# Optimization experiments

Hardware: AMD Instinct MI355X
Metric: run time of the kernel (lower is better)

## Reference

```python
import jax, jax.numpy as jnp
import numpy as np

H = 8
HID = 512
DH = HID // H
EPS = 1e-5


def _ln(x, g, b):
    mu = jnp.mean(x, axis=-1, keepdims=True)
    var = jnp.mean(jnp.square(x - mu), axis=-1, keepdims=True)
    return (x - mu) * jax.lax.rsqrt(var + EPS) * g + b


def setup_inputs() -> dict:
    key = jax.random.key(0)
    ks = jax.random.split(key, 40)
    L, M, P, D = 4096, 1024, 4096, 512

    def xav(k, shp):
        lim = np.sqrt(6.0 / (shp[0] + shp[1]))
        return jax.random.uniform(k, shp, jnp.float32, -lim, lim)

    inp = {
        'lncRNA_embedding': jax.random.normal(ks[0], (L, D), jnp.float32),
        'miRNA_embedding': jax.random.normal(ks[1], (M, D), jnp.float32),
        'protein_embedding': jax.random.normal(ks[2], (P, D), jnp.float32),
        'lncRNA_miRNA_matrix': jax.random.randint(ks[3], (L, M), 0, 2, jnp.int32),
        'protein_miRNA_matrix': jax.random.randint(ks[4], (P, M), 0, 2, jnp.int32),
    }
    names = ['Wl', 'Wm', 'Wp', 'Wql', 'Wkl', 'Wvl', 'Wqp', 'Wkp', 'Wvp']
    for i, n in enumerate(names):
        inp[n] = xav(ks[5 + i], (HID, HID))
        inp['b' + n[1:]] = jnp.zeros((HID,), jnp.float32)
    inp['Wml'] = xav(ks[20], (2 * HID, D // 2))
    inp['bml'] = jnp.zeros((D // 2,), jnp.float32)
    inp['Wmp'] = xav(ks[21], (2 * HID, D // 2))
    inp['bmp'] = jnp.zeros((D // 2,), jnp.float32)
    inp['g1'] = jnp.ones((D // 2,), jnp.float32)
    inp['be1'] = jnp.zeros((D // 2,), jnp.float32)
    inp['g2'] = jnp.ones((D // 2,), jnp.float32)
    inp['be2'] = jnp.zeros((D // 2,), jnp.float32)
    # first three linears take dim-D input (D == HID here)
    return inp


def reference(lncRNA_embedding, miRNA_embedding, protein_embedding,
              lncRNA_miRNA_matrix, protein_miRNA_matrix,
              Wl, bl, Wm, bm, Wp, bp,
              Wql, bql, Wkl, bkl, Wvl, bvl,
              Wqp, bqp, Wkp, bkp, Wvp, bvp,
              Wml, bml, Wmp, bmp, g1, be1, g2, be2):
    L = lncRNA_embedding.shape[0]
    M = miRNA_embedding.shape[0]
    P = protein_embedding.shape[0]

    lt = lncRNA_embedding @ Wl + bl          # [L, HID]
    mt = miRNA_embedding @ Wm + bm           # [M, HID]
    pt = protein_embedding @ Wp + bp         # [P, HID]

    def heads(x, W, b, n):
        return (x @ W + b).reshape(n, H, DH)

    Ql = heads(lt, Wql, bql, L)              # [L, H, DH]
    Kl = heads(mt, Wkl, bkl, M)
    Vl = heads(mt, Wvl, bvl, M)
    Qp = heads(pt, Wqp, bqp, P)
    Kp = heads(mt, Wkp, bkp, M)
    Vp = heads(mt, Wvp, bvp, M)

    scale = 1.0 / np.sqrt(DH)
    sl = jnp.einsum('lhd,mhd->hlm', Ql, Kl) * scale      # [H, L, M]
    sl = jnp.where(lncRNA_miRNA_matrix[None] == 0, -1e9, sl)
    awl = jax.nn.softmax(sl, axis=-1)

    sp = jnp.einsum('phd,mhd->hpm', Qp, Kp) * scale      # [H, P, M]
    sp = jnp.where(protein_miRNA_matrix[None] == 0, -1e9, sp)
    awp = jax.nn.softmax(sp, axis=-1)

    ctx_l = jax.nn.relu(jnp.einsum('hlm,mhd->lhd', awl, Vl).reshape(L, HID))
    ctx_p = jax.nn.relu(jnp.einsum('hpm,mhd->phd', awp, Vp).reshape(P, HID))

    mutual = jnp.einsum('hlm,hpm->lp', awl, awp) / H     # [L, P]

    fin_l = ctx_l + mutual @ ctx_p
    fin_p = ctx_p + mutual.T @ ctx_l

    out_l = _ln(jnp.concatenate([lt, fin_l], axis=-1) @ Wml + bml, g1, be1)
    out_p = _ln(jnp.concatenate([fin_p, pt], axis=-1) @ Wmp + bmp, g2, be2)
    return out_l, out_p
```

## Files before the change

kernel.cpp:

```cpp
#include <hip/hip_runtime.h>
#include <hip/hip_bf16.h>

using bf16 = __hip_bfloat16;
typedef __attribute__((ext_vector_type(8))) short short8;
typedef __attribute__((ext_vector_type(4))) float floatx4;
typedef __attribute__((ext_vector_type(8))) unsigned short ushort8;
typedef __attribute__((ext_vector_type(4))) int i32x4;
typedef __attribute__((ext_vector_type(8))) int i32x8;

__device__ __forceinline__ float b2f(unsigned short u) {
    union { unsigned int i; float f; } x; x.i = ((unsigned int)u) << 16; return x.f;
}

__device__ __forceinline__ void async16(const void* g, void* l) {
    __builtin_amdgcn_global_load_lds((const __attribute__((address_space(1))) void*)g,
                                     (__attribute__((address_space(3))) void*)l,
                                     16, 0, 0);
}

__device__ __forceinline__ unsigned char f2e4m3(float f) {
    unsigned s = (__float_as_uint(f) >> 24) & 0x80u;
    f = fminf(fabsf(f), 448.f);
    if (f < 0.015625f) {
        int d = (int)rintf(f * 512.f);
        return (unsigned char)(s | (unsigned)d);
    }
    int E = (int)((__float_as_uint(f) >> 23) & 255u) - 127;
    float ulp_inv = __uint_as_float((unsigned)(127 + 3 - E) << 23);
    int m = (int)rintf(f * ulp_inv);
    int n = (m == 16) ? ((E + 8) << 3) : (((E + 7) << 3) + (m - 8));
    if (n > 0x7E) n = 0x7E;
    return (unsigned char)(s | (unsigned)n);
}

__device__ __forceinline__ bool sniff_wave(const unsigned short* p) {
    const int lane = threadIdx.x & 63;
    int wild = 0;
#pragma unroll
    for (int j = 0; j < 4; ++j) {
        float a = fabsf(b2f(p[lane * 4 + j]));
        wild += !(a <= 1e4f);
    }
#pragma unroll
    for (int o = 1; o < 64; o <<= 1) wild += __shfl_xor(wild, o);
    return wild > 16;
}

struct Cvt { const void* src; bf16* dst; int n; };
struct PrepArgs {
    Cvt cv[18];
    const void* tsrc[11];
    bf16* tdst[11];
    const unsigned short* sn;
};

__global__ __launch_bounds__(256) void prep(PrepArgs a) {
    const bool f32 = sniff_wave(a.sn);
    const int y = blockIdx.y;
    __shared__ bf16 tile[32][33];

    if (y < 18) {
        const Cvt c = a.cv[y];
        const int stride = gridDim.x * 256 * 8;
        for (int i = (blockIdx.x * 256 + threadIdx.x) * 8; i < c.n; i += stride) {
            if (f32) {
                const float* s = (const float*)c.src + i;
#pragma unroll
                for (int j = 0; j < 8; ++j) c.dst[i + j] = __float2bfloat16(s[j]);
            } else {
                *(ushort8*)((unsigned short*)c.dst + i) =
                    *(const ushort8*)((const unsigned short*)c.src + i);
            }
        }
        return;
    }

    const int tx = threadIdx.x & 31;
    const int ty = threadIdx.x >> 5;
    if (y < 27) {
        const void* in = a.tsrc[y - 18];
        bf16* out = a.tdst[y - 18];
        const int bc = (blockIdx.x & 15) * 32;
        const int br = (blockIdx.x >> 4) * 32;
#pragma unroll
        for (int i = 0; i < 32; i += 8) {
            const size_t idx = (size_t)(br + ty + i) * 512 + bc + tx;
            tile[ty + i][tx] = f32 ? __float2bfloat16(((const float*)in)[idx])
                                   : ((const bf16*)in)[idx];
        }
        __syncthreads();
#pragma unroll
        for (int i = 0; i < 32; i += 8)
            out[(size_t)(bc + ty + i) * 512 + br + tx] = tile[tx][ty + i];
    } else {
        const void* in = a.tsrc[y - 27 + 9];
        bf16* out = a.tdst[y - 27 + 9];
        const int bc = (blockIdx.x & 7) * 32;
        const int br = (blockIdx.x >> 3) * 32;
#pragma unroll
        for (int i = 0; i < 32; i += 8) {
            const size_t idx = (size_t)(br + ty + i) * 256 + bc + tx;
            tile[ty + i][tx] = f32 ? __float2bfloat16(((const float*)in)[idx])
                                   : ((const bf16*)in)[idx];
        }
        __syncthreads();
#pragma unroll
        for (int i = 0; i < 32; i += 8)
            out[(size_t)(bc + ty + i) * 1024 + br + tx] = tile[tx][ty + i];
    }
}

struct SegTab { const bf16* W[3]; const bf16* bias[3]; bf16* C[3]; int ldc[3]; int rs[3]; };

__global__ __launch_bounds__(256) void gemm_bt_seg(
    const bf16* __restrict__ A, SegTab T, int K)
{
    constexpr int TM = 2, TN = 2;
    __align__(16) __shared__ bf16 As[64 * 64];
    __align__(16) __shared__ bf16 Bs[64 * 64];

    const int lane = threadIdx.x & 63;
    const int wv   = threadIdx.x >> 6;
    const int gm   = blockIdx.y * 64;
    const int seg  = (gm >= 5120) ? 2 : ((gm >= 4096) ? 1 : 0);
    const bf16* B  = T.W[seg];
    const bf16* bias = T.bias[seg];
    bf16* C        = T.C[seg];
    const int ldc  = T.ldc[seg];
    const int m_base = gm - T.rs[seg];
    const int n_base = blockIdx.x * 64;
    const int wm0 = (wv >> 1) * 32;
    const int wn0 = (wv & 1) * 32;

    floatx4 zero = {0.f, 0.f, 0.f, 0.f};
    floatx4 acc[TM][TN];
#pragma unroll
    for (int mt = 0; mt < TM; ++mt)
#pragma unroll
        for (int nt = 0; nt < TN; ++nt) acc[mt][nt] = zero;

    const int sr  = lane >> 3;
    const int sce = ((lane & 7) ^ sr) * 8;
    const int fr  = lane & 15;
    const int q   = lane >> 4;
    const int sw  = fr & 7;

    for (int k0 = 0; k0 < K; k0 += 64) {
#pragma unroll
        for (int cc = 0; cc < 2; ++cc) {
            const int r0t = (wv + cc * 4) * 8;
            async16(A + (size_t)(gm + r0t + sr) * 512 + k0 + sce, &As[r0t * 64]);
            async16(B + (size_t)(n_base + r0t + sr) * 512 + k0 + sce, &Bs[r0t * 64]);
        }
        __syncthreads();
#pragma unroll
        for (int s = 0; s < 2; ++s) {
            const int off = ((s * 4 + q) ^ sw) * 8;
            short8 af[TM], bfr[TN];
#pragma unroll
            for (int mt = 0; mt < TM; ++mt)
                af[mt] = *(const short8*)&As[(wm0 + mt * 16 + fr) * 64 + off];
#pragma unroll
            for (int nt = 0; nt < TN; ++nt)
                bfr[nt] = *(const short8*)&Bs[(wn0 + nt * 16 + fr) * 64 + off];
#pragma unroll
            for (int mt = 0; mt < TM; ++mt)
#pragma unroll
                for (int nt = 0; nt < TN; ++nt)
                    acc[mt][nt] = __builtin_amdgcn_mfma_f32_16x16x32_bf16(
                        af[mt], bfr[nt], acc[mt][nt], 0, 0, 0);
        }
        __syncthreads();
    }

    const int er = lane >> 4;
    const int ec = lane & 15;
#pragma unroll
    for (int nt = 0; nt < TN; ++nt) {
        const int col = n_base + wn0 + nt * 16 + ec;
        const float bv = __bfloat162float(bias[col]);
#pragma unroll
        for (int mt = 0; mt < TM; ++mt)
#pragma unroll
            for (int r = 0; r < 4; ++r) {
                const int row = m_base + wm0 + mt * 16 + er * 4 + r;
                C[(size_t)row * ldc + col] = __float2bfloat16(acc[mt][nt][r] + bv);
            }
    }
}

struct BtArgs { const bf16* A; const bf16* B; void* C; const bf16* bias;
                int lda, ldb, ldc; };
struct BtSet { BtArgs s[3]; };

template <bool F32OUT, bool REMAP2>
__global__ __launch_bounds__(256) void gemm_btx(BtSet P, int K, float scale)
{
    constexpr int TM = 2, TN = 2;
    __align__(16) __shared__ bf16 As[64 * 64];
    __align__(16) __shared__ bf16 Bs[64 * 64];

    const BtArgs g = P.s[blockIdx.z];
    int bx = blockIdx.x, by = blockIdx.y;
    if (REMAP2 && blockIdx.z == 2) {
        const int flat = by * gridDim.x + bx;
        bx = flat & 31; by = flat >> 5;
    }
    const int lane = threadIdx.x & 63;
    const int wv   = threadIdx.x >> 6;
    const int m_base = by * 64;
    const int n_base = bx * 64;
    const int wm0 = (wv >> 1) * 32;
    const int wn0 = (wv & 1) * 32;

    floatx4 zero = {0.f, 0.f, 0.f, 0.f};
    floatx4 acc[TM][TN];
#pragma unroll
    for (int mt = 0; mt < TM; ++mt)
#pragma unroll
        for (int nt = 0; nt < TN; ++nt) acc[mt][nt] = zero;

    const int sr  = lane >> 3;
    const int sce = ((lane & 7) ^ sr) * 8;
    const int fr  = lane & 15;
    const int q   = lane >> 4;
    const int sw  = fr & 7;

    for (int k0 = 0; k0 < K; k0 += 64) {
#pragma unroll
        for (int cc = 0; cc < 2; ++cc) {
            const int r0t = (wv + cc * 4) * 8;
            async16(g.A + (size_t)(m_base + r0t + sr) * g.lda + k0 + sce, &As[r0t * 64]);
            async16(g.B + (size_t)(n_base + r0t + sr) * g.ldb + k0 + sce, &Bs[r0t * 64]);
        }
        __syncthreads();
#pragma unroll
        for (int s = 0; s < 2; ++s) {
            const int off = ((s * 4 + q) ^ sw) * 8;
            short8 af[TM], bfr[TN];
#pragma unroll
            for (int mt = 0; mt < TM; ++mt)
                af[mt] = *(const short8*)&As[(wm0 + mt * 16 + fr) * 64 + off];
#pragma unroll
            for (int nt = 0; nt < TN; ++nt)
                bfr[nt] = *(const short8*)&Bs[(wn0 + nt * 16 + fr) * 64 + off];
#pragma unroll
            for (int mt = 0; mt < TM; ++mt)
#pragma unroll
                for (int nt = 0; nt < TN; ++nt)
                    acc[mt][nt] = __builtin_amdgcn_mfma_f32_16x16x32_bf16(
                        af[mt], bfr[nt], acc[mt][nt], 0, 0, 0);
        }
        __syncthreads();
    }

    const int er = lane >> 4;
    const int ec = lane & 15;
#pragma unroll
    for (int nt = 0; nt < TN; ++nt) {
        const int col = n_base + wn0 + nt * 16 + ec;
        const float bv = __bfloat162float(g.bias[col]);
#pragma unroll
        for (int mt = 0; mt < TM; ++mt)
#pragma unroll
            for (int r = 0; r < 4; ++r) {
                const int row = m_base + wm0 + mt * 16 + er * 4 + r;
                const float v = acc[mt][nt][r] * scale + bv;
                if constexpr (F32OUT)
                    ((float*)g.C)[(size_t)row * g.ldc + col] = v;
                else
                    ((bf16*)g.C)[(size_t)row * g.ldc + col] = __float2bfloat16(v);
            }
    }
}

struct ScArgs { const bf16* Q; const bf16* K; const int* mask; unsigned char* aw; };
struct ScSet { ScArgs s[2]; const bf16* vsrc[2]; unsigned char* vdst[2]; };

__global__ __launch_bounds__(256) void scores_v8(ScSet P, int ldk, float scale)
{
    __shared__ float wred[16][4];
    __shared__ float wsum[16][4];
    __shared__ float tile[32][33];

    if (blockIdx.z == 2) {
        const int flat = blockIdx.y * 256 + blockIdx.x;
        if (flat >= 1024) return;
        const int side = flat >> 9;
        const int rem  = flat & 511;
        const bf16* in = P.vsrc[side];
        unsigned char* out = P.vdst[side];
        const int bc = (rem & 15) * 32;
        const int br = (rem >> 4) * 32;
        const int tx = threadIdx.x & 31;
        const int ty = threadIdx.x >> 5;
#pragma unroll
        for (int i = 0; i < 32; i += 8)
            tile[ty + i][tx] =
                __bfloat162float(in[(size_t)(br + ty + i) * 2048 + bc + tx]) * 4.0f;
        __syncthreads();
#pragma unroll
        for (int i = 0; i < 32; i += 8)
            out[(size_t)(bc + ty + i) * 1024 + br + tx] = f2e4m3(tile[tx][ty + i]);
        return;
    }

    const ScArgs g = P.s[blockIdx.z];
    const int t    = threadIdx.x;
    const int lane = t & 63;
    const int w    = t >> 6;
    const int h    = blockIdx.y;
    const int r0   = blockIdx.x * 16;
    const int fr   = lane & 15;
    const int fq   = lane >> 4;
    const int cbase = w * 256;

    const short* Qs = (const short*)g.Q + (size_t)(r0 + fr) * 512 + h * 64 + fq * 8;
    short8 a0 = *(const short8*)(Qs);
    short8 a1 = *(const short8*)(Qs + 32);

    floatx4 accs[16];
    const short* Kb = (const short*)g.K + h * 64 + fq * 8;
#pragma unroll
    for (int c = 0; c < 16; ++c) {
        const int krow = cbase + c * 16 + fr;
        short8 b0 = *(const short8*)(Kb + (size_t)krow * ldk);
        short8 b1 = *(const short8*)(Kb + (size_t)krow * ldk + 32);
        floatx4 acc = {0.f, 0.f, 0.f, 0.f};
        acc = __builtin_amdgcn_mfma_f32_16x16x32_bf16(a0, b0, acc, 0, 0, 0);
        acc = __builtin_amdgcn_mfma_f32_16x16x32_bf16(a1, b1, acc, 0, 0, 0);
        accs[c] = acc;
    }

    float mxr[4] = {-3e38f, -3e38f, -3e38f, -3e38f};
#pragma unroll
    for (int c = 0; c < 16; ++c) {
        const int col = cbase + c * 16 + fr;
#pragma unroll
        for (int r = 0; r < 4; ++r) {
            const int row = r0 + fq * 4 + r;
            float v = (g.mask[(size_t)row * 1024 + col] == 0) ? -1e9f
                                                              : accs[c][r] * scale;
            accs[c][r] = v;
            mxr[r] = fmaxf(mxr[r], v);
        }
    }
#pragma unroll
    for (int o = 1; o < 16; o <<= 1)
#pragma unroll
        for (int r = 0; r < 4; ++r) mxr[r] = fmaxf(mxr[r], __shfl_xor(mxr[r], o));
    if (fr == 0)
#pragma unroll
        for (int r = 0; r < 4; ++r) wred[fq * 4 + r][w] = mxr[r];
    __syncthreads();

    float mx[4], sm[4] = {0.f, 0.f, 0.f, 0.f};
#pragma unroll
    for (int r = 0; r < 4; ++r) {
        const int row = fq * 4 + r;
        mx[r] = fmaxf(fmaxf(wred[row][0], wred[row][1]),
                      fmaxf(wred[row][2], wred[row][3]));
    }
#pragma unroll
    for (int c = 0; c < 16; ++c)
#pragma unroll
        for (int r = 0; r < 4; ++r) {
            float e = __expf(accs[c][r] - mx[r]);
            accs[c][r] = e;
            sm[r] += e;
        }
#pragma unroll
    for (int o = 1; o < 16; o <<= 1)
#pragma unroll
        for (int r = 0; r < 4; ++r) sm[r] += __shfl_xor(sm[r], o);
    if (fr == 0)
#pragma unroll
        for (int r = 0; r < 4; ++r) wsum[fq * 4 + r][w] = sm[r];
    __syncthreads();

    float inv[4];
#pragma unroll
    for (int r = 0; r < 4; ++r) {
        const int row = fq * 4 + r;
        inv[r] = 32.0f / (wsum[row][0] + wsum[row][1] + wsum[row][2] + wsum[row][3]);
    }
#pragma unroll
    for (int c = 0; c < 16; ++c) {
        const int col = cbase + c * 16 + fr;
#pragma unroll
        for (int r = 0; r < 4; ++r) {
            const int row = r0 + fq * 4 + r;
            g.aw[(size_t)row * 8192 + h * 1024 + col] = f2e4m3(accs[c][r] * inv[r]);
        }
    }
}

struct B8Args { const unsigned char* A; const unsigned char* B; bf16* C;
                unsigned char* CT; };
struct B8Pair { B8Args s[2]; };

__global__ __launch_bounds__(256) void gemm_bt8_ctx(
    B8Pair P, int lda, long long a_kshift, int ldb, int ldc, int ldct,
    int K, float scale)
{
    constexpr int TM = 2, TN = 2;
    __align__(16) __shared__ unsigned char As[64 * 64];
    __align__(16) __shared__ unsigned char Bs[64 * 64];

    const B8Args g = P.s[blockIdx.z];
    const int lane = threadIdx.x & 63;
    const int wv   = threadIdx.x >> 6;
    const int m_base = blockIdx.y * 64;
    const int n_base = blockIdx.x * 64;
    const unsigned char* A = g.A + (long long)blockIdx.x * a_kshift;

    const int wm0 = (wv >> 1) * 32;
    const int wn0 = (wv & 1) * 32;

    floatx4 zero = {0.f, 0.f, 0.f, 0.f};
    floatx4 acc[TM][TN];
#pragma unroll
    for (int mt = 0; mt < TM; ++mt)
#pragma unroll
        for (int nt = 0; nt < TN; ++nt) acc[mt][nt] = zero;

    const int ar = lane >> 2;
    const int ac = (((lane & 3) ^ (ar & 3)) * 16);
    const int fr = lane & 15;
    const int q  = lane >> 4;
    const int sw = fr & 3;

    for (int k0 = 0; k0 < K; k0 += 64) {
        async16(A + (size_t)(m_base + wv * 16 + ar) * lda + k0 + ac, &As[wv * 16 * 64]);
        async16(g.B + (size_t)(n_base + wv * 16 + ar) * ldb + k0 + ac, &Bs[wv * 16 * 64]);
        __syncthreads();
#pragma unroll
        for (int s = 0; s < 2; ++s) {
            const int boff = (((s * 2 + (q >> 1)) ^ sw) * 16) + (q & 1) * 8;
            long af[TM], bfr[TN];
#pragma unroll
            for (int mt = 0; mt < TM; ++mt)
                af[mt] = *(const long*)&As[(wm0 + mt * 16 + fr) * 64 + boff];
#pragma unroll
            for (int nt = 0; nt < TN; ++nt)
                bfr[nt] = *(const long*)&Bs[(wn0 + nt * 16 + fr) * 64 + boff];
#pragma unroll
            for (int mt = 0; mt < TM; ++mt)
#pragma unroll
                for (int nt = 0; nt < TN; ++nt)
                    acc[mt][nt] = __builtin_amdgcn_mfma_f32_16x16x32_fp8_fp8(
                        af[mt], bfr[nt], acc[mt][nt], 0, 0, 0);
        }
        __syncthreads();
    }

    const int er = lane >> 4;
    const int ec = lane & 15;
#pragma unroll
    for (int nt = 0; nt < TN; ++nt) {
        const int col = n_base + wn0 + nt * 16 + ec;
#pragma unroll
        for (int mt = 0; mt < TM; ++mt) {
            const int rowb = m_base + wm0 + mt * 16 + er * 4;
            unsigned int pk = 0;
#pragma unroll
            for (int r = 0; r < 4; ++r) {
                float v = fmaxf(acc[mt][nt][r] * scale, 0.f);
                g.C[(size_t)(rowb + r) * ldc + col] = __float2bfloat16(v);
                pk |= (unsigned)f2e4m3(v * 16.0f) << (8 * r);
            }
            *(unsigned int*)(g.CT + (size_t)col * ldct + rowb) = pk;
        }
    }
}

struct MxArgs { const unsigned char* A; const unsigned char* B; void* C;
                const bf16* Cz; unsigned char* CT; };
struct MxPair { MxArgs s[2]; };

template <int BM, int BN, bool ADDC0, bool FP8OUT, bool TOUT>
__global__ __launch_bounds__(256, 2) void gemm_bt8mx(
    MxPair P, int lda, int ldb, int ldc, int ldc0, int ldct, int K, float scale)
{
    constexpr int WM = BM / 2;
    constexpr int WN = BN / 2;
    constexpr int TM = WM / 16;
    constexpr int TN = WN / 16;

    __align__(16) __shared__ unsigned char As[BM * 128];
    __align__(16) __shared__ unsigned char Bs[BN * 128];

    const MxArgs g = P.s[blockIdx.z];
    const int lane = threadIdx.x & 63;
    const int wv   = threadIdx.x >> 6;
    const int m_base = blockIdx.y * BM;
    const int n_base = blockIdx.x * BN;

    const int wm0 = (wv >> 1) * WM;
    const int wn0 = (wv & 1) * WN;

    floatx4 zero = {0.f, 0.f, 0.f, 0.f};
    floatx4 acc[TM][TN];
#pragma unroll
    for (int mt = 0; mt < TM; ++mt)
#pragma unroll
        for (int nt = 0; nt < TN; ++nt) acc[mt][nt] = zero;

    const int sr = lane >> 3;
    const int sc = ((lane & 7) ^ sr) * 16;
    const int fr = lane & 15;
    const int q  = lane >> 4;
    const int sw = fr & 7;

    for (int k0 = 0; k0 < K; k0 += 128) {
#pragma unroll
        for (int cc = 0; cc < BM / 32; ++cc) {
            const int r0t = (wv + cc * 4) * 8;
            async16(g.A + (size_t)(m_base + r0t + sr) * lda + k0 + sc, &As[r0t * 128]);
        }
#pragma unroll
        for (int cc = 0; cc < BN / 32; ++cc) {
            const int r0t = (wv + cc * 4) * 8;
            async16(g.B + (size_t)(n_base + r0t + sr) * ldb + k0 + sc, &Bs[r0t * 128]);
        }
        __syncthreads();

        i32x8 af[TM];
#pragma unroll
        for (int mt = 0; mt < TM; ++mt) {
            const unsigned char* rp = &As[(wm0 + mt * 16 + fr) * 128];
            i32x4 lo = *(const i32x4*)(rp + (((q * 2 + 0) ^ sw) * 16));
            i32x4 hi = *(const i32x4*)(rp + (((q * 2 + 1) ^ sw) * 16));
            af[mt] = __builtin_shufflevector(lo, hi, 0, 1, 2, 3, 4, 5, 6, 7);
        }
#pragma unroll
        for (int nt = 0; nt < TN; ++nt) {
            const unsigned char* rp = &Bs[(wn0 + nt * 16 + fr) * 128];
            i32x4 lo = *(const i32x4*)(rp + (((q * 2 + 0) ^ sw) * 16));
            i32x4 hi = *(const i32x4*)(rp + (((q * 2 + 1) ^ sw) * 16));
            i32x8 bf8 = __builtin_shufflevector(lo, hi, 0, 1, 2, 3, 4, 5, 6, 7);
#pragma unroll
            for (int mt = 0; mt < TM; ++mt)
                acc[mt][nt] = __builtin_amdgcn_mfma_scale_f32_16x16x128_f8f6f4(
                    af[mt], bf8, acc[mt][nt], 0, 0, 0, 127, 0, 127);
        }
        __syncthreads();
    }

    const int er = lane >> 4;
    const int ec = lane & 15;
#pragma unroll
    for (int nt = 0; nt < TN; ++nt) {
        const int col = n_base + wn0 + nt * 16 + ec;
#pragma unroll
        for (int mt = 0; mt < TM; ++mt) {
            const int rowb = m_base + wm0 + mt * 16 + er * 4;
            unsigned int pk = 0;
#pragma unroll
            for (int r = 0; r < 4; ++r) {
                float v = acc[mt][nt][r] * scale;
                if constexpr (ADDC0)
                    v += __bfloat162float(g.Cz[(size_t)(rowb + r) * ldc0 + col]);
                if constexpr (FP8OUT) {
                    const unsigned char qv = f2e4m3(v);
                    ((unsigned char*)g.C)[(size_t)(rowb + r) * ldc + col] = qv;
                    if constexpr (TOUT) pk |= (unsigned)qv << (8 * r);
                } else {
                    ((bf16*)g.C)[(size_t)(rowb + r) * ldc + col] = __float2bfloat16(v);
                }
            }
            if constexpr (TOUT)
                *(unsigned int*)(g.CT + (size_t)col * ldct + rowb) = pk;
        }
    }
}

__global__ __launch_bounds__(256) void ln_all(
    const float* __restrict__ X,
    const bf16* __restrict__ g1, const bf16* __restrict__ be1,
    const bf16* __restrict__ g2, const bf16* __restrict__ be2,
    void* __restrict__ out, const unsigned short* __restrict__ sn)
{
    const bool f32 = sniff_wave(sn);
    const int lane = threadIdx.x & 63;
    const int wv   = threadIdx.x >> 6;
    const int row  = blockIdx.x * 4 + wv;
    const bf16* gg = (row >= 4096) ? g2 : g1;
    const bf16* bb = (row >= 4096) ? be2 : be1;
    const float* x = X + (size_t)row * 256;
    float v[4], s = 0.f, s2 = 0.f;
#pragma unroll
    for (int i = 0; i < 4; ++i) {
        v[i] = x[lane + 64 * i];
        s += v[i]; s2 += v[i] * v[i];
    }
#pragma unroll
    for (int o = 1; o < 64; o <<= 1) { s += __shfl_xor(s, o); s2 += __shfl_xor(s2, o); }
    const float mu  = s * (1.0f / 256.0f);
    const float var = fmaxf(s2 * (1.0f / 256.0f) - mu * mu, 0.0f);
    const float inv = rsqrtf(var + 1e-5f);
#pragma unroll
    for (int i = 0; i < 4; ++i) {
        const int c = lane + 64 * i;
        const float y = (v[i] - mu) * inv * __bfloat162float(gg[c]) + __bfloat162float(bb[c]);
        if (f32) ((float*)out)[(size_t)row * 256 + c] = y;
        else     ((bf16*)out)[(size_t)row * 256 + c] = __float2bfloat16(y);
    }
}

extern "C" void kernel_launch(void* const* d_in, const int* in_sizes, int n_in,
                              void* d_out, int out_size, void* d_ws, size_t ws_size,
                              hipStream_t stream)
{
    const int L = 4096, Mm = 1024, P = 4096;

    const int* mask_l = (const int*)d_in[3];
    const int* mask_p = (const int*)d_in[4];
    const unsigned short* sn = (const unsigned short*)d_in[0];

    char* ws = (char*)d_ws;
    size_t off = 0;
    auto alloc = [&](size_t bytes) {
        void* p = ws + off; off += (bytes + 255) & ~(size_t)255; return p;
    };

    bf16* wt_all = (bf16*)alloc((size_t)9 * 512 * 512 * 2);
    bf16* WmlT   = (bf16*)alloc(1024 * 256 * 2);
    bf16* WmpT   = (bf16*)alloc(1024 * 256 * 2);
    bf16* b_l    = (bf16*)alloc(512 * 2);
    bf16* b_m    = (bf16*)alloc(512 * 2);
    bf16* b_p    = (bf16*)alloc(512 * 2);
    bf16* b_ql   = (bf16*)alloc(512 * 2);
    bf16* b_qp   = (bf16*)alloc(512 * 2);
    bf16* bcat   = (bf16*)alloc(2048 * 2);
    bf16* bml_c  = (bf16*)alloc(256 * 2);
    bf16* bmp_c  = (bf16*)alloc(256 * 2);
    bf16* g1c    = (bf16*)alloc(256 * 2);
    bf16* be1c   = (bf16*)alloc(256 * 2);
    bf16* g2c    = (bf16*)alloc(256 * 2);
    bf16* be2c   = (bf16*)alloc(256 * 2);
    bf16* emb_all = (bf16*)alloc((size_t)(L + Mm + P) * 512 * 2);
    bf16* embl   = emb_all;
    bf16* embm   = emb_all + (size_t)L * 512;
    bf16* embp   = embm + (size_t)Mm * 512;
    bf16* cat_l  = (bf16*)alloc((size_t)L * 1024 * 2);
    bf16* cat_p  = (bf16*)alloc((size_t)P * 1024 * 2);
    bf16* mt     = (bf16*)alloc((size_t)Mm * 512 * 2);
    bf16* Ql     = (bf16*)alloc((size_t)L * 512 * 2);
    bf16* Qp     = (bf16*)alloc((size_t)P * 512 * 2);
    bf16* kvcat  = (bf16*)alloc((size_t)Mm * 2048 * 2);
    unsigned char* V8lT = (unsigned char*)alloc((size_t)512 * Mm);
    unsigned char* V8pT = (unsigned char*)alloc((size_t)512 * Mm);
    bf16* ctx_l  = (bf16*)alloc((size_t)L * 512 * 2);
    bf16* ctx_p  = (bf16*)alloc((size_t)P * 512 * 2);
    unsigned char* ctx8lT = (unsigned char*)alloc((size_t)512 * L);
    unsigned char* ctx8pT = (unsigned char*)alloc((size_t)512 * P);
    unsigned char* mutual8  = (unsigned char*)alloc((size_t)L * P);
    unsigned char* mutual8T = (unsigned char*)alloc((size_t)L * P);
    unsigned char* awl8 = (unsigned char*)alloc((size_t)L * 8192);
    unsigned char* awp8 = (unsigned char*)alloc((size_t)P * 8192);
    float* tmp1 = (float*)awp8;

    PrepArgs pa;
    pa.sn = sn;
    pa.cv[0]  = { d_in[0],  embl, L * 512 };
    pa.cv[1]  = { d_in[1],  embm, Mm * 512 };
    pa.cv[2]  = { d_in[2],  embp, P * 512 };
    pa.cv[3]  = { d_in[6],  b_l,  512 };
    pa.cv[4]  = { d_in[8],  b_m,  512 };
    pa.cv[5]  = { d_in[10], b_p,  512 };
    pa.cv[6]  = { d_in[12], b_ql, 512 };
    pa.cv[7]  = { d_in[18], b_qp, 512 };
    pa.cv[8]  = { d_in[14], bcat,        512 };
    pa.cv[9]  = { d_in[16], bcat + 512,  512 };
    pa.cv[10] = { d_in[20], bcat + 1024, 512 };
    pa.cv[11] = { d_in[22], bcat + 1536, 512 };
    pa.cv[12] = { d_in[24], bml_c, 256 };
    pa.cv[13] = { d_in[26], bmp_c, 256 };
    pa.cv[14] = { d_in[27], g1c,  256 };
    pa.cv[15] = { d_in[28], be1c, 256 };
    pa.cv[16] = { d_in[29], g2c,  256 };
    pa.cv[17] = { d_in[30], be2c, 256 };
    const int slot_of[9] = {0, 1, 2, 3, 5, 6, 4, 7, 8};
    for (int i = 0; i < 9; ++i) {
        pa.tsrc[i] = d_in[5 + 2 * i];
        pa.tdst[i] = wt_all + (size_t)slot_of[i] * 512 * 512;
    }
    pa.tsrc[9]  = d_in[23]; pa.tdst[9]  = WmlT;
    pa.tsrc[10] = d_in[25]; pa.tdst[10] = WmpT;
    prep<<<dim3(256, 29), 256, 0, stream>>>(pa);

    bf16* WlT  = wt_all;
    bf16* WmT  = wt_all + (size_t)1 * 512 * 512;
    bf16* WpT  = wt_all + (size_t)2 * 512 * 512;
    bf16* WqlT = wt_all + (size_t)3 * 512 * 512;
    bf16* WqpT = wt_all + (size_t)4 * 512 * 512;
    bf16* WkvT = wt_all + (size_t)5 * 512 * 512;

    SegTab st;
    st.W[0] = WlT;  st.bias[0] = b_l; st.C[0] = cat_l;       st.ldc[0] = 1024; st.rs[0] = 0;
    st.W[1] = WmT;  st.bias[1] = b_m; st.C[1] = mt;          st.ldc[1] = 512;  st.rs[1] = 4096;
    st.W[2] = WpT;  st.bias[2] = b_p; st.C[2] = cat_p + 512; st.ldc[2] = 1024; st.rs[2] = 5120;
    gemm_bt_seg<<<dim3(8, 144), 256, 0, stream>>>(emb_all, st, 512);

    BtSet qs;
    qs.s[0] = { cat_l,       WqlT, Ql,    b_ql, 1024, 512, 512 };
    qs.s[1] = { cat_p + 512, WqpT, Qp,    b_qp, 1024, 512, 512 };
    qs.s[2] = { mt,          WkvT, kvcat, bcat, 512,  512, 2048 };
    gemm_btx<false, true><<<dim3(8, 64, 3), 256, 0, stream>>>(qs, 512, 1.0f);

    ScSet sc;
    sc.s[0] = { Ql, kvcat,        mask_l, awl8 };
    sc.s[1] = { Qp, kvcat + 1024, mask_p, awp8 };
    sc.vsrc[0] = kvcat + 512;  sc.vdst[0] = V8lT;
    sc.vsrc[1] = kvcat + 1536; sc.vdst[1] = V8pT;
    scores_v8<<<dim3(256, 8, 3), 256, 0, stream>>>(sc, 2048, 0.125f);

    B8Pair cx = { { { awl8, V8lT, ctx_l, ctx8lT },
                    { awp8, V8pT, ctx_p, ctx8pT } } };
    gemm_bt8_ctx<<<dim3(8, 64, 2), 256, 0, stream>>>(
        cx, 8192, 1024, 1024, 512, 4096, 1024, 1.0f / 128.0f);

    MxPair mu = { { { awl8, awp8, mutual8, nullptr, mutual8T },
                    { awl8, awp8, mutual8, nullptr, mutual8T } } };
    gemm_bt8mx<256, 128, false, true, true><<<dim3(32, 16, 1), 256, 0, stream>>>(
        mu, 8192, 8192, 4096, 0, 4096, 8192, 0.03125f);

    MxPair fn = { { { mutual8,  ctx8pT, cat_l + 512, ctx_l, nullptr },
                    { mutual8T, ctx8lT, cat_p,       ctx_p, nullptr } } };
    gemm_bt8mx<64, 128, true, false, false><<<dim3(4, 64, 2), 256, 0, stream>>>(
        fn, 4096, 4096, 1024, 512, 0, 4096, 1.0f / 4096.0f);

    BtSet fp;
    fp.s[0] = { cat_l, WmlT, tmp1,                   bml_c, 1024, 1024, 256 };
    fp.s[1] = { cat_p, WmpT, tmp1 + (size_t)L * 256, bmp_c, 1024, 1024, 256 };
    fp.s[2] = fp.s[0];
    gemm_btx<true, false><<<dim3(4, 64, 2), 256, 0, stream>>>(fp, 1024, 1.0f);

    ln_all<<<dim3(2048), 256, 0, stream>>>(tmp1, g1c, be1c, g2c, be2c, d_out, sn);
}
```

Measured before the change: 507.7 us.

## Add dedicated double-buffered 512-thread FP8 kernel for mutual attention GEMM

Replaces the generic templated MX-FP8 GEMM used for the L×P mutual-attention product with a specialized kernel. It uses 8 waves (512 threads) with 64x64 warp tiles, double-buffered LDS tiles filled by async global-to-LDS loads that overlap with MFMA compute, and s_setprio around the MFMA block. The goal is to hide global load latency and raise MFMA utilization on the largest GEMM (K=8192). The cost is doubled LDS use (96KB per block), which may limit occupancy, plus hardcoded 4096 leading dimensions.

```diff
diff --git a/kernel.cpp b/kernel.cpp
--- a/kernel.cpp
+++ b/kernel.cpp
@@ -470,6 +470,106 @@
                 pk |= (unsigned)f2e4m3(v * 16.0f) << (8 * r);
             }
             *(unsigned int*)(g.CT + (size_t)col * ldct + rowb) = pk;
+        }
+    }
+}
+
+__global__ __launch_bounds__(512, 2) void gemm_mutual(
+    const unsigned char* __restrict__ A, const unsigned char* __restrict__ B,
+    unsigned char* __restrict__ C, unsigned char* __restrict__ CT,
+    int K, float scale)
+{
+    constexpr int BM = 256, BN = 128;
+    constexpr int TM = 4, TN = 4;
+
+    __align__(16) __shared__ unsigned char As[2][BM * 128];
+    __align__(16) __shared__ unsigned char Bs[2][BN * 128];
+
+    const int lane = threadIdx.x & 63;
+    const int wv   = threadIdx.x >> 6;
+    const int m_base = blockIdx.y * BM;
+    const int n_base = blockIdx.x * BN;
+    const int wm0 = (wv >> 1) * 64;
+    const int wn0 = (wv & 1) * 64;
+
+    floatx4 zero = {0.f, 0.f, 0.f, 0.f};
+    floatx4 acc[TM][TN];
+#pragma unroll
+    for (int mt = 0; mt < TM; ++mt)
+#pragma unroll
+        for (int nt = 0; nt < TN; ++nt) acc[mt][nt] = zero;
+
+    const int sr = lane >> 3;
+    const int sc = ((lane & 7) ^ sr) * 16;
+    const int fr = lane & 15;
+    const int q  = lane >> 4;
+    const int sw = fr & 7;
+
+    const int NT = K >> 7;
+
+    auto stage = [&](int t, int b) {
+        const int k0 = t << 7;
+#pragma unroll
+        for (int cc = 0; cc < 4; ++cc) {
+            const int r0t = (wv + cc * 8) * 8;
+            async16(A + (size_t)(m_base + r0t + sr) * (size_t)K + k0 + sc,
+                    &As[b][r0t * 128]);
+        }
+#pragma unroll
+        for (int cc = 0; cc < 2; ++cc) {
+            const int r0t = (wv + cc * 8) * 8;
+            async16(B + (size_t)(n_base + r0t + sr) * (size_t)K + k0 + sc,
+                    &Bs[b][r0t * 128]);
+        }
+    };
+
+    stage(0, 0);
+    asm volatile("s_waitcnt vmcnt(0)\n\ts_barrier" ::: "memory");
+
+    for (int t = 0; t < NT; ++t) {
+        const int cur = t & 1;
+        if (t + 1 < NT) stage(t + 1, cur ^ 1);
+
+        i32x8 af[TM];
+#pragma unroll
+        for (int mt = 0; mt < TM; ++mt) {
+            const unsigned char* rp = &As[cur][(wm0 + mt * 16 + fr) * 128];
+            i32x4 lo = *(const i32x4*)(rp + (((q * 2 + 0) ^ sw) * 16));
+            i32x4 hi = *(const i32x4*)(rp + (((q * 2 + 1) ^ sw) * 16));
+            af[mt] = __builtin_shufflevector(lo, hi, 0, 1, 2, 3, 4, 5, 6, 7);
+        }
+        __builtin_amdgcn_s_setprio(1);
+#pragma unroll
+        for (int nt = 0; nt < TN; ++nt) {
+            const unsigned char* rp = &Bs[cur][(wn0 + nt * 16 + fr) * 128];
+            i32x4 lo = *(const i32x4*)(rp + (((q * 2 + 0) ^ sw) * 16));
+            i32x4 hi = *(const i32x4*)(rp + (((q * 2 + 1) ^ sw) * 16));
+            i32x8 bf8 = __builtin_shufflevector(lo, hi, 0, 1, 2, 3, 4, 5, 6, 7);
+#pragma unroll
+            for (int mt = 0; mt < TM; ++mt)
+                acc[mt][nt] = __builtin_amdgcn_mfma_scale_f32_16x16x128_f8f6f4(
+                    af[mt], bf8, acc[mt][nt], 0, 0, 0, 127, 0, 127);
+        }
+        __builtin_amdgcn_s_setprio(0);
+        asm volatile("s_waitcnt vmcnt(0)\n\ts_barrier" ::: "memory");
+    }
+
+    const int er = lane >> 4;
+    const int ec = lane & 15;
+#pragma unroll
+    for (int nt = 0; nt < TN; ++nt) {
+        const int col = n_base + wn0 + nt * 16 + ec;
+#pragma unroll
+        for (int mt = 0; mt < TM; ++mt) {
+            const int rowb = m_base + wm0 + mt * 16 + er * 4;
+            unsigned int pk = 0;
+#pragma unroll
+            for (int r = 0; r < 4; ++r) {
+                const unsigned char qv = f2e4m3(acc[mt][nt][r] * scale);
+                C[(size_t)(rowb + r) * 4096 + col] = qv;
+                pk |= (unsigned)qv << (8 * r);
+            }
+            *(unsigned int*)(CT + (size_t)col * 4096 + rowb) = pk;
         }
     }
 }
@@ -721,10 +821,8 @@
     gemm_bt8_ctx<<<dim3(8, 64, 2), 256, 0, stream>>>(
         cx, 8192, 1024, 1024, 512, 4096, 1024, 1.0f / 128.0f);
 
-    MxPair mu = { { { awl8, awp8, mutual8, nullptr, mutual8T },
-                    { awl8, awp8, mutual8, nullptr, mutual8T } } };
-    gemm_bt8mx<256, 128, false, true, true><<<dim3(32, 16, 1), 256, 0, stream>>>(
-        mu, 8192, 8192, 4096, 0, 4096, 8192, 0.03125f);
+    gemm_mutual<<<dim3(32, 16), 512, 0, stream>>>(
+        awl8, awp8, mutual8, mutual8T, 8192, 0.03125f);
 
     MxPair fn = { { { mutual8,  ctx8pT, cat_l + 512, ctx_l, nullptr },
                     { mutual8T, ctx8lT, cat_p,       ctx_p, nullptr } } };
```

New measurement: 564.8 us. 11.2% more time.

## Reassociate mutual-attention product to avoid materializing the L×P mutual matrix

Applied to the files above, without the earlier changes.

Instead of computing mutual = awl·awpᵀ (L×P, K=8192) and then mutual·ctx_p, the code first computes T1 = awpᵀ-side product with ctx (512×8192) and then multiplies awl by T1, reassociating the matrix chain. The scores kernel now also writes a transposed fp8 copy of the attention weights so the new GEMMs can read them in the needed layout. This cuts the FLOPs of the mutual path (L·P·8192 + L·P·512 becomes roughly 2·512·8192·4096 per side) at the cost of extra transposed stores from the scores kernel and larger scratch buffers, and changes the fp8 quantization points.

```diff
diff --git a/kernel.cpp b/kernel.cpp
--- a/kernel.cpp
+++ b/kernel.cpp
@@ -274,7 +274,8 @@
     }
 }
 
-struct ScArgs { const bf16* Q; const bf16* K; const int* mask; unsigned char* aw; };
+struct ScArgs { const bf16* Q; const bf16* K; const int* mask; unsigned char* aw;
+                unsigned char* awt; };
 struct ScSet { ScArgs s[2]; const bf16* vsrc[2]; unsigned char* vdst[2]; };
 
 __global__ __launch_bounds__(256) void scores_v8(ScSet P, int ldk, float scale)
@@ -387,11 +388,15 @@
 #pragma unroll
     for (int c = 0; c < 16; ++c) {
         const int col = cbase + c * 16 + fr;
+        unsigned int pk = 0;
 #pragma unroll
         for (int r = 0; r < 4; ++r) {
             const int row = r0 + fq * 4 + r;
-            g.aw[(size_t)row * 8192 + h * 1024 + col] = f2e4m3(accs[c][r] * inv[r]);
-        }
+            const unsigned char qv = f2e4m3(accs[c][r] * inv[r]);
+            g.aw[(size_t)row * 8192 + h * 1024 + col] = qv;
+            pk |= (unsigned)qv << (8 * r);
+        }
+        *(unsigned int*)(g.awt + (size_t)(h * 1024 + col) * 4096 + r0 + fq * 4) = pk;
     }
 }
 
@@ -655,10 +660,12 @@
     bf16* ctx_p  = (bf16*)alloc((size_t)P * 512 * 2);
     unsigned char* ctx8lT = (unsigned char*)alloc((size_t)512 * L);
     unsigned char* ctx8pT = (unsigned char*)alloc((size_t)512 * P);
-    unsigned char* mutual8  = (unsigned char*)alloc((size_t)L * P);
-    unsigned char* mutual8T = (unsigned char*)alloc((size_t)L * P);
+    unsigned char* awlT8  = (unsigned char*)alloc((size_t)8192 * 4096);
+    unsigned char* awpT8  = (unsigned char*)alloc((size_t)8192 * 4096);
     unsigned char* awl8 = (unsigned char*)alloc((size_t)L * 8192);
     unsigned char* awp8 = (unsigned char*)alloc((size_t)P * 8192);
+    unsigned char* T1lT = (unsigned char*)emb_all;
+    unsigned char* T1pT = (unsigned char*)emb_all + (size_t)512 * 8192;
     float* tmp1 = (float*)awp8;
 
     PrepArgs pa;
@@ -710,8 +717,8 @@
     gemm_btx<false, true><<<dim3(8, 64, 3), 256, 0, stream>>>(qs, 512, 1.0f);
 
     ScSet sc;
-    sc.s[0] = { Ql, kvcat,        mask_l, awl8 };
-    sc.s[1] = { Qp, kvcat + 1024, mask_p, awp8 };
+    sc.s[0] = { Ql, kvcat,        mask_l, awl8, awlT8 };
+    sc.s[1] = { Qp, kvcat + 1024, mask_p, awp8, awpT8 };
     sc.vsrc[0] = kvcat + 512;  sc.vdst[0] = V8lT;
     sc.vsrc[1] = kvcat + 1536; sc.vdst[1] = V8pT;
     scores_v8<<<dim3(256, 8, 3), 256, 0, stream>>>(sc, 2048, 0.125f);
@@ -721,15 +728,15 @@
     gemm_bt8_ctx<<<dim3(8, 64, 2), 256, 0, stream>>>(
         cx, 8192, 1024, 1024, 512, 4096, 1024, 1.0f / 128.0f);
 
-    MxPair mu = { { { awl8, awp8, mutual8, nullptr, mutual8T },
-                    { awl8, awp8, mutual8, nullptr, mutual8T } } };
-    gemm_bt8mx<256, 128, false, true, true><<<dim3(32, 16, 1), 256, 0, stream>>>(
-        mu, 8192, 8192, 4096, 0, 4096, 8192, 0.03125f);
-
-    MxPair fn = { { { mutual8,  ctx8pT, cat_l + 512, ctx_l, nullptr },
-                    { mutual8T, ctx8lT, cat_p,       ctx_p, nullptr } } };
-    gemm_bt8mx<64, 128, true, false, false><<<dim3(4, 64, 2), 256, 0, stream>>>(
-        fn, 4096, 4096, 1024, 512, 0, 4096, 1.0f / 4096.0f);
+    MxPair t1 = { { { ctx8pT, awpT8, T1lT, nullptr, nullptr },
+                    { ctx8lT, awlT8, T1pT, nullptr, nullptr } } };
+    gemm_bt8mx<128, 256, false, true, false><<<dim3(32, 4, 2), 256, 0, stream>>>(
+        t1, 4096, 4096, 8192, 0, 0, 4096, 1.0f / 128.0f);
+
+    MxPair fn = { { { awl8, T1lT, cat_l + 512, ctx_l, nullptr },
+                    { awp8, T1pT, cat_p,       ctx_p, nullptr } } };
+    gemm_bt8mx<128, 128, true, false, false><<<dim3(4, 32, 2), 256, 0, stream>>>(
+        fn, 8192, 8192, 1024, 512, 0, 8192, 1.0f / 1024.0f);
 
     BtSet fp;
     fp.s[0] = { cat_l, WmlT, tmp1,                   bml_c, 1024, 1024, 256 };
```

Measured after the change: 516.7 us. No clear change (+1.8%).
